# Performance work log

Hardware: AMD Instinct MI355X
Metric: run time of the kernel (lower is better)

## Reference

```python
import jax, jax.numpy as jnp
import numpy as np

B, N, RIN, ROUT, DEMB, FIN, FE, E, ITERS = 64, 128, 32, 64, 64, 64, 16, 65536, 3
NTOT = B * N


def gnn(x, edge_index, edge_feat, Ws, Wm, We, b):
    # edge-conditioned message passing: [NTOT, Fin] -> [NTOT, Fout]
    src, dst = edge_index[0], edge_index[1]
    msg = jax.nn.relu(x[src] @ Wm + edge_feat @ We)          # [E, Fout]
    agg = jax.ops.segment_sum(msg, dst, num_segments=x.shape[0])
    return jax.nn.relu(x @ Ws + agg + b)


def setup_inputs() -> dict:
    key = jax.random.key(0)
    ks = jax.random.split(key, 20)
    s = 0.1
    return {
        "x_r": jax.random.normal(ks[0], (NTOT, FIN), jnp.float32),
        "edge_index_r": jax.random.randint(ks[1], (2, E), 0, NTOT),
        "edge_feat_r": jax.random.normal(ks[2], (E, FE), jnp.float32),
        "x_p": jax.random.normal(ks[3], (NTOT, FIN), jnp.float32),
        "edge_index_p": jax.random.randint(ks[4], (2, E), 0, NTOT),
        "edge_feat_p": jax.random.normal(ks[5], (E, FE), jnp.float32),
        "r_mask": jnp.ones((B, N), dtype=bool),
        "p_mask": jnp.ones((B, N), dtype=bool),
        # gnn_1 params (FIN -> DEMB)
        "g1_Ws": jax.random.normal(ks[6], (FIN, DEMB)) * s,
        "g1_Wm": jax.random.normal(ks[7], (FIN, DEMB)) * s,
        "g1_We": jax.random.normal(ks[8], (FE, DEMB)) * s,
        "g1_b": jnp.zeros((DEMB,), jnp.float32),
        # gnn_2 params (RIN -> ROUT)
        "g2_Ws": jax.random.normal(ks[9], (RIN, ROUT)) * s,
        "g2_Wm": jax.random.normal(ks[10], (RIN, ROUT)) * s,
        "g2_We": jax.random.normal(ks[11], (FE, ROUT)) * s,
        "g2_b": jnp.zeros((ROUT,), jnp.float32),
        # consensus mlp (ROUT -> ROUT -> 1)
        "mlp_W1": jax.random.normal(ks[12], (ROUT, ROUT)) * s,
        "mlp_b1": jnp.zeros((ROUT,), jnp.float32),
        "mlp_W2": jax.random.normal(ks[13], (ROUT, 1)) * s,
        "mlp_b2": jnp.zeros((1,), jnp.float32),
    }


def reference(x_r, edge_index_r, edge_feat_r, x_p, edge_index_p, edge_feat_p,
              r_mask, p_mask,
              g1_Ws, g1_Wm, g1_We, g1_b,
              g2_Ws, g2_Wm, g2_We, g2_b,
              mlp_W1, mlp_b1, mlp_W2, mlp_b2):
    # node embeddings via gnn_1, then dense-batch to [B, N, DEMB]
    h_r = gnn(x_r, edge_index_r, edge_feat_r, g1_Ws, g1_Wm, g1_We, g1_b).reshape(B, N, DEMB)
    h_p = gnn(x_p, edge_index_p, edge_feat_p, g1_Ws, g1_Wm, g1_We, g1_b).reshape(B, N, DEMB)

    M_hat = jnp.einsum('brd,bpd->brp', h_r, h_p)             # [B, N_r, N_p]
    M_mask = r_mask[:, :, None] & p_mask[:, None, :]
    M_0 = jax.nn.softmax(M_hat, axis=-1).reshape(NTOT, N)    # packed (full mask)

    rkey = jax.random.key(42)
    for it in range(ITERS):
        M = jax.nn.softmax(M_hat, axis=-1)
        rf_r = jax.random.normal(jax.random.fold_in(rkey, it), (B, N, RIN), jnp.float32)
        rf_p = jnp.einsum('brp,bri->bpi', M, rf_r)           # M^T @ rand
        o_r = gnn(rf_r.reshape(NTOT, RIN), edge_index_r, edge_feat_r,
                  g2_Ws, g2_Wm, g2_We, g2_b).reshape(B, N, ROUT)
        o_p = gnn(rf_p.reshape(NTOT, RIN), edge_index_p, edge_feat_p,
                  g2_Ws, g2_Wm, g2_We, g2_b).reshape(B, N, ROUT)
        D = o_r[:, :, None, :] - o_p[:, None, :, :]          # [B, N_r, N_p, ROUT]
        upd = (jax.nn.relu(D @ mlp_W1 + mlp_b1) @ mlp_W2 + mlp_b2)[..., 0]
        M_hat = M_hat + jnp.where(M_mask, upd, 0.0)

    M_T = jax.nn.softmax(M_hat, axis=-1).reshape(NTOT, N)
    return (M_0, M_T)
```

## Files before the change

kernel.cpp:

```cpp
#include <hip/hip_runtime.h>

constexpr int kE = 65536, kNTOT = 8192;

__host__ __device__ __forceinline__ void tf_round(unsigned& x0, unsigned& x1, int r) {
  x0 += x1;
  x1 = (x1 << r) | (x1 >> (32 - r));
  x1 ^= x0;
}
__host__ __device__ __forceinline__ void tf2x32(unsigned k0, unsigned k1,
                                                unsigned& x0, unsigned& x1) {
  unsigned ks2 = k0 ^ k1 ^ 0x1BD11BDAu;
  x0 += k0; x1 += k1;
  tf_round(x0,x1,13); tf_round(x0,x1,15); tf_round(x0,x1,26); tf_round(x0,x1,6);
  x0 += k1; x1 += ks2 + 1u;
  tf_round(x0,x1,17); tf_round(x0,x1,29); tf_round(x0,x1,16); tf_round(x0,x1,24);
  x0 += ks2; x1 += k0 + 2u;
  tf_round(x0,x1,13); tf_round(x0,x1,15); tf_round(x0,x1,26); tf_round(x0,x1,6);
  x0 += k0; x1 += k1 + 3u;
  tf_round(x0,x1,17); tf_round(x0,x1,29); tf_round(x0,x1,16); tf_round(x0,x1,24);
  x0 += k1; x1 += ks2 + 4u;
  tf_round(x0,x1,13); tf_round(x0,x1,15); tf_round(x0,x1,26); tf_round(x0,x1,6);
  x0 += ks2; x1 += k0 + 5u;
}

__device__ __forceinline__ float bits_to_normal(unsigned bits) {
  float f = __uint_as_float((bits >> 9) | 0x3f800000u) - 1.0f;
  const float LO = -0.99999994f;
  float u = fmaf(f, 2.0f, LO);
  u = fmaxf(u, LO);
  float w = -log1pf(-u * u);
  float p;
  if (w < 5.0f) {
    w -= 2.5f;
    p = 2.81022636e-08f;
    p = fmaf(p, w, 3.43273939e-07f);
    p = fmaf(p, w, -3.5233877e-06f);
    p = fmaf(p, w, -4.39150654e-06f);
    p = fmaf(p, w, 0.00021858087f);
    p = fmaf(p, w, -0.00125372503f);
    p = fmaf(p, w, -0.00417768164f);
    p = fmaf(p, w, 0.246640727f);
    p = fmaf(p, w, 1.50140941f);
  } else {
    w = sqrtf(w) - 3.0f;
    p = -0.000200214257f;
    p = fmaf(p, w, 0.000100950558f);
    p = fmaf(p, w, 0.00134934322f);
    p = fmaf(p, w, -0.00367342844f);
    p = fmaf(p, w, 0.00573950773f);
    p = fmaf(p, w, -0.0076224613f);
    p = fmaf(p, w, 0.00943887047f);
    p = fmaf(p, w, 1.00167406f);
    p = fmaf(p, w, 2.83297682f);
  }
  return 1.41421356f * (p * u);
}

__device__ __forceinline__ float redmax32(float v) {
#pragma unroll
  for (int o = 16; o > 0; o >>= 1) v = fmaxf(v, __shfl_xor(v, o));
  return v;
}
__device__ __forceinline__ float redsum32(float v) {
#pragma unroll
  for (int o = 16; o > 0; o >>= 1) v += __shfl_xor(v, o);
  return v;
}

__global__ __launch_bounds__(256) void hist_kern(const int* __restrict__ eiR,
                                                 const int* __restrict__ eiP,
                                                 int* __restrict__ cntR,
                                                 int* __restrict__ cntP,
                                                 float* __restrict__ aggz) {
  int i = blockIdx.x * 256 + threadIdx.x;
  float4 z4 = make_float4(0.f, 0.f, 0.f, 0.f);
  float4* z = reinterpret_cast<float4*>(aggz) + i * 2;
  z[0] = z4; z[1] = z4;
  const int* ei = (i < kE) ? eiR : eiP;
  int* cnt = (i < kE) ? cntR : cntP;
  int e = i & (kE - 1);
  atomicAdd(&cnt[ei[kE + e]], 1);
}

__global__ __launch_bounds__(256) void scan_kern(const int* __restrict__ cntR,
                                                 int* __restrict__ rpR, int* __restrict__ offR,
                                                 const int* __restrict__ cntP,
                                                 int* __restrict__ rpP, int* __restrict__ offP) {
  const int* cnt = blockIdx.x ? cntP : cntR;
  int* rp = blockIdx.x ? rpP : rpR;
  int* off = blockIdx.x ? offP : offR;
  int t = threadIdx.x;
  int base = t * 32;
  int v[32];
#pragma unroll
  for (int i = 0; i < 32; ++i) v[i] = cnt[base + i];
  int sum = 0;
#pragma unroll
  for (int i = 0; i < 32; ++i) sum += v[i];
  int lane = t & 63, w = t >> 6;
  int incl = sum;
#pragma unroll
  for (int o = 1; o < 64; o <<= 1) {
    int y = __shfl_up(incl, o);
    if (lane >= o) incl += y;
  }
  __shared__ int wsum[4];
  if (lane == 63) wsum[w] = incl;
  __syncthreads();
  int woff = 0;
#pragma unroll
  for (int i = 0; i < 4; ++i) if (i < w) woff += wsum[i];
  int running = woff + incl - sum;
#pragma unroll
  for (int i = 0; i < 32; ++i) {
    rp[base + i] = running;
    off[base + i] = running;
    running += v[i];
  }
  if (t == 0) rp[kNTOT] = kE;
}

__global__ __launch_bounds__(256) void scatter_kern(
    const int* __restrict__ eiR, const int* __restrict__ eiP,
    int* __restrict__ offR, int* __restrict__ offP,
    int* __restrict__ permR, int* __restrict__ permP,
    int* __restrict__ srcsR, int* __restrict__ srcsP,
    int* __restrict__ dstsR, int* __restrict__ dstsP) {
  int i = blockIdx.x * 256 + threadIdx.x;
  const int* ei = (i < kE) ? eiR : eiP;
  int* off = (i < kE) ? offR : offP;
  int* perm = (i < kE) ? permR : permP;
  int* srcs = (i < kE) ? srcsR : srcsP;
  int* dsts = (i < kE) ? dstsR : dstsP;
  int e = i & (kE - 1);
  int dst = ei[kE + e];
  int pos = atomicAdd(&off[dst], 1);
  perm[pos] = e;
  srcs[pos] = ei[e];
  dsts[pos] = dst;
}

template <int KX>
__global__ __launch_bounds__(256) void msg_gemm(
    const float* __restrict__ xR, const float* __restrict__ efR,
    const int* __restrict__ srcsR, const int* __restrict__ permR,
    const int* __restrict__ dstsR, float* __restrict__ aggR,
    const float* __restrict__ xP, const float* __restrict__ efP,
    const int* __restrict__ srcsP, const int* __restrict__ permP,
    const int* __restrict__ dstsP, float* __restrict__ aggP,
    const float* __restrict__ Wm, const float* __restrict__ We) {
  constexpr int KT = KX + 16;
  constexpr int SA_ROWS = (KT > 64) ? KT : 64;
  __shared__ float sA[SA_ROWS][68];
  __shared__ float sW[KT][68];
  __shared__ int sDst[64];
  bool isP = blockIdx.x >= 1024;
  const float* x = isP ? xP : xR;
  const float* ef = isP ? efP : efR;
  const int* srcs = isP ? srcsP : srcsR;
  const int* perm = isP ? permP : permR;
  const int* dsts = isP ? dstsP : dstsR;
  float* agg = isP ? aggP : aggR;
  int i0 = (blockIdx.x & 1023) * 64;
  int t = threadIdx.x;
#pragma unroll
  for (int idx = 0; idx < KT * 64 / 1024; ++idx) {
    int q = t * 4 + idx * 1024;
    int k = q >> 6, j = q & 63;
    const float* sp = (k < KX) ? (Wm + k * 64 + j) : (We + (k - KX) * 64 + j);
    float4 v = *reinterpret_cast<const float4*>(sp);
    *reinterpret_cast<float4*>(&sW[k][j]) = v;
  }
  if (t < 64) sDst[t] = dsts[i0 + t];
#pragma unroll
  for (int idx = 0; idx < KT * 64 / 1024; ++idx) {
    int q = t * 4 + idx * 1024;
    int r = q / KT;
    int k = q % KT;
    const float* rptr = (k < KX) ? (x + (size_t)srcs[i0 + r] * KX + k)
                                 : (ef + (size_t)perm[i0 + r] * 16 + (k - KX));
    float4 v = *reinterpret_cast<const float4*>(rptr);
    sA[k + 0][r] = v.x; sA[k + 1][r] = v.y; sA[k + 2][r] = v.z; sA[k + 3][r] = v.w;
  }
  __syncthreads();
  int tn = (t & 15) * 4;
  int tj = (t >> 4) * 4;
  float acc[4][4] = {};
#pragma unroll 8
  for (int k = 0; k < KT; ++k) {
    float4 a = *reinterpret_cast<const float4*>(&sA[k][tn]);
    float4 b = *reinterpret_cast<const float4*>(&sW[k][tj]);
    acc[0][0] = fmaf(a.x, b.x, acc[0][0]); acc[0][1] = fmaf(a.x, b.y, acc[0][1]);
    acc[0][2] = fmaf(a.x, b.z, acc[0][2]); acc[0][3] = fmaf(a.x, b.w, acc[0][3]);
    acc[1][0] = fmaf(a.y, b.x, acc[1][0]); acc[1][1] = fmaf(a.y, b.y, acc[1][1]);
    acc[1][2] = fmaf(a.y, b.z, acc[1][2]); acc[1][3] = fmaf(a.y, b.w, acc[1][3]);
    acc[2][0] = fmaf(a.z, b.x, acc[2][0]); acc[2][1] = fmaf(a.z, b.y, acc[2][1]);
    acc[2][2] = fmaf(a.z, b.z, acc[2][2]); acc[2][3] = fmaf(a.z, b.w, acc[2][3]);
    acc[3][0] = fmaf(a.w, b.x, acc[3][0]); acc[3][1] = fmaf(a.w, b.y, acc[3][1]);
    acc[3][2] = fmaf(a.w, b.z, acc[3][2]); acc[3][3] = fmaf(a.w, b.w, acc[3][3]);
  }
  __syncthreads();
#pragma unroll
  for (int i = 0; i < 4; ++i) {
    sA[tn + i][tj + 0] = fmaxf(acc[i][0], 0.f);
    sA[tn + i][tj + 1] = fmaxf(acc[i][1], 0.f);
    sA[tn + i][tj + 2] = fmaxf(acc[i][2], 0.f);
    sA[tn + i][tj + 3] = fmaxf(acc[i][3], 0.f);
  }
  __syncthreads();
  int col = t & 63;
  int r0l = (t >> 6) * 16;
  float run = 0.f;
  int rd = sDst[r0l];
#pragma unroll
  for (int r = 0; r < 16; ++r) {
    int d = sDst[r0l + r];
    if (d != rd) {
      unsafeAtomicAdd(&agg[(size_t)rd * 64 + col], run);
      run = 0.f; rd = d;
    }
    run += sA[r0l + r][col];
  }
  unsafeAtomicAdd(&agg[(size_t)rd * 64 + col], run);
}

__global__ __launch_bounds__(256) void node1_gemm(
    const float* __restrict__ xR, float* __restrict__ aggR, float* __restrict__ hR,
    const float* __restrict__ xP, float* __restrict__ aggP, float* __restrict__ hP,
    const float* __restrict__ Ws, const float* __restrict__ bias) {
  __shared__ float sX[64][68];
  __shared__ float sW[64][68];
  bool isP = blockIdx.x >= 128;
  const float* x = isP ? xP : xR;
  float* agg = isP ? aggP : aggR;
  float* h = isP ? hP : hR;
  int n0 = (blockIdx.x & 127) * 64;
  int t = threadIdx.x;
#pragma unroll
  for (int idx = 0; idx < 4; ++idx) {
    int q = t * 4 + idx * 1024;
    int k = q >> 6, j = q & 63;
    *reinterpret_cast<float4*>(&sW[k][j]) = *reinterpret_cast<const float4*>(Ws + q);
    float4 v = *reinterpret_cast<const float4*>(x + (size_t)n0 * 64 + q);
    sX[j + 0][k] = v.x; sX[j + 1][k] = v.y; sX[j + 2][k] = v.z; sX[j + 3][k] = v.w;
  }
  __syncthreads();
  int tn = (t & 15) * 4, tj = (t >> 4) * 4;
  float acc[4][4] = {};
#pragma unroll 8
  for (int k = 0; k < 64; ++k) {
    float4 a = *reinterpret_cast<const float4*>(&sX[k][tn]);
    float4 b = *reinterpret_cast<const float4*>(&sW[k][tj]);
    acc[0][0] = fmaf(a.x, b.x, acc[0][0]); acc[0][1] = fmaf(a.x, b.y, acc[0][1]);
    acc[0][2] = fmaf(a.x, b.z, acc[0][2]); acc[0][3] = fmaf(a.x, b.w, acc[0][3]);
    acc[1][0] = fmaf(a.y, b.x, acc[1][0]); acc[1][1] = fmaf(a.y, b.y, acc[1][1]);
    acc[1][2] = fmaf(a.y, b.z, acc[1][2]); acc[1][3] = fmaf(a.y, b.w, acc[1][3]);
    acc[2][0] = fmaf(a.z, b.x, acc[2][0]); acc[2][1] = fmaf(a.z, b.y, acc[2][1]);
    acc[2][2] = fmaf(a.z, b.z, acc[2][2]); acc[2][3] = fmaf(a.z, b.w, acc[2][3]);
    acc[3][0] = fmaf(a.w, b.x, acc[3][0]); acc[3][1] = fmaf(a.w, b.y, acc[3][1]);
    acc[3][2] = fmaf(a.w, b.z, acc[3][2]); acc[3][3] = fmaf(a.w, b.w, acc[3][3]);
  }
  float4 bv = *reinterpret_cast<const float4*>(bias + tj);
  float4 z4 = make_float4(0.f, 0.f, 0.f, 0.f);
#pragma unroll
  for (int i = 0; i < 4; ++i) {
    int n = n0 + tn + i;
    float4 g = *reinterpret_cast<const float4*>(&agg[(size_t)n * 64 + tj]);
    *reinterpret_cast<float4*>(&agg[(size_t)n * 64 + tj]) = z4;
    float4 o;
    o.x = fmaxf(acc[i][0] + g.x + bv.x, 0.f);
    o.y = fmaxf(acc[i][1] + g.y + bv.y, 0.f);
    o.z = fmaxf(acc[i][2] + g.z + bv.z, 0.f);
    o.w = fmaxf(acc[i][3] + g.w + bv.w, 0.f);
    *reinterpret_cast<float4*>(&h[(size_t)n * 64 + tj]) = o;
  }
}

__global__ __launch_bounds__(256) void mhat_soft(
    const float* __restrict__ hR, const float* __restrict__ hP,
    float* __restrict__ Mhat, float* __restrict__ Msoft, float* __restrict__ M0out,
    float* __restrict__ rfr, unsigned fk0, unsigned fk1) {
  __shared__ float hr[16][66];
  __shared__ float hp[128][66];
  int gid = blockIdx.x, t = threadIdx.x;
  int gtid = (gid << 8) + t;
#pragma unroll
  for (int q = 0; q < 2; ++q) {
    unsigned i = (unsigned)gtid + (unsigned)q * 131072u;
    unsigned a0 = 0u, a1 = i;
    tf2x32(fk0, fk1, a0, a1);
    rfr[i] = bits_to_normal(a0 ^ a1);
  }
  int b = gid >> 3, r0 = (gid & 7) * 16;
  const float* hrG = hR + ((size_t)(b * 128 + r0)) * 64;
  {
    int q = t * 4; int r = q >> 6, d = q & 63;
    float4 v = *reinterpret_cast<const float4*>(hrG + q);
    hr[r][d] = v.x; hr[r][d + 1] = v.y; hr[r][d + 2] = v.z; hr[r][d + 3] = v.w;
  }
  const float* hpG = hP + (size_t)b * 128 * 64;
#pragma unroll
  for (int rep = 0; rep < 8; ++rep) {
    int q = (rep * 256 + t) * 4; int p = q >> 6, d = q & 63;
    float4 v = *reinterpret_cast<const float4*>(hpG + q);
    hp[p][d] = v.x; hp[p][d + 1] = v.y; hp[p][d + 2] = v.z; hp[p][d + 3] = v.w;
  }
  __syncthreads();
  int tx = t & 31, ty = t >> 5;
  float acc[2][4] = {};
  for (int d = 0; d < 64; ++d) {
    float a0 = hr[ty][d], a1 = hr[ty + 8][d];
    float q0 = hp[tx][d], q1 = hp[tx + 32][d], q2 = hp[tx + 64][d], q3 = hp[tx + 96][d];
    acc[0][0] = fmaf(a0, q0, acc[0][0]); acc[0][1] = fmaf(a0, q1, acc[0][1]);
    acc[0][2] = fmaf(a0, q2, acc[0][2]); acc[0][3] = fmaf(a0, q3, acc[0][3]);
    acc[1][0] = fmaf(a1, q0, acc[1][0]); acc[1][1] = fmaf(a1, q1, acc[1][1]);
    acc[1][2] = fmaf(a1, q2, acc[1][2]); acc[1][3] = fmaf(a1, q3, acc[1][3]);
  }
#pragma unroll
  for (int ii = 0; ii < 2; ++ii) {
    int r = r0 + ty + 8 * ii;
    float* mrow = Mhat + ((size_t)(b * 128 + r)) * 128;
    mrow[tx] = acc[ii][0]; mrow[tx + 32] = acc[ii][1];
    mrow[tx + 64] = acc[ii][2]; mrow[tx + 96] = acc[ii][3];
    float mx = redmax32(fmaxf(fmaxf(acc[ii][0], acc[ii][1]), fmaxf(acc[ii][2], acc[ii][3])));
    float e0 = __expf(acc[ii][0] - mx), e1 = __expf(acc[ii][1] - mx);
    float e2 = __expf(acc[ii][2] - mx), e3 = __expf(acc[ii][3] - mx);
    float inv = 1.0f / redsum32(e0 + e1 + e2 + e3);
    float* srow = Msoft + ((size_t)(b * 128 + r)) * 128;
    srow[tx] = e0 * inv; srow[tx + 32] = e1 * inv;
    srow[tx + 64] = e2 * inv; srow[tx + 96] = e3 * inv;
    float* orow = M0out + ((size_t)(b * 128 + r)) * 128;
    orow[tx] = e0 * inv; orow[tx + 32] = e1 * inv;
    orow[tx + 64] = e2 * inv; orow[tx + 96] = e3 * inv;
  }
}

__global__ __launch_bounds__(256) void rfp_kern(
    const float* __restrict__ Msoft, const float* __restrict__ rfr,
    float* __restrict__ rfp) {
  __shared__ float rr[128][36];
  int b = blockIdx.x >> 3, p0 = (blockIdx.x & 7) * 16;
  int t = threadIdx.x;
  const float* rfG = rfr + (size_t)b * 4096;
#pragma unroll
  for (int rep = 0; rep < 4; ++rep) {
    int q = (rep * 256 + t) * 4; int r = q >> 5, i = q & 31;
    float4 v = *reinterpret_cast<const float4*>(rfG + q);
    rr[r][i] = v.x; rr[r][i + 1] = v.y; rr[r][i + 2] = v.z; rr[r][i + 3] = v.w;
  }
  __syncthreads();
  int pl = t & 15, ih = (t >> 4) * 2;
  int p = p0 + pl;
  const float* Mcol = Msoft + (size_t)b * 16384 + p;
  float a0 = 0.f, a1 = 0.f;
#pragma unroll 8
  for (int r = 0; r < 128; ++r) {
    float m = Mcol[(size_t)r * 128];
    a0 = fmaf(m, rr[r][ih], a0);
    a1 = fmaf(m, rr[r][ih + 1], a1);
  }
  float* dst = rfp + ((size_t)(b * 128 + p)) * 32 + ih;
  dst[0] = a0; dst[1] = a1;
}

__global__ __launch_bounds__(256) void node2u_gemm(
    const float* __restrict__ rfR, float* __restrict__ aggR, float* __restrict__ uR,
    const float* __restrict__ rfP, float* __restrict__ aggP, float* __restrict__ uP,
    const float* __restrict__ Ws2, const float* __restrict__ g2b,
    const float* __restrict__ W1, const float* __restrict__ b1) {
  __shared__ float sRF[32][68];
  __shared__ float sW2[32][68];
  __shared__ float sW1[64][68];
  __shared__ float sO[64][68];
  bool isP = blockIdx.x >= 128;
  const float* rf = isP ? rfP : rfR;
  float* agg = isP ? aggP : aggR;
  float* u = isP ? uP : uR;
  int n0 = (blockIdx.x & 127) * 64;
  int t = threadIdx.x;
#pragma unroll
  for (int idx = 0; idx < 4; ++idx) {
    int q = t * 4 + idx * 1024;
    *reinterpret_cast<float4*>(&sW1[q >> 6][q & 63]) = *reinterpret_cast<const float4*>(W1 + q);
  }
#pragma unroll
  for (int idx = 0; idx < 2; ++idx) {
    int q = t * 4 + idx * 1024;
    *reinterpret_cast<float4*>(&sW2[q >> 6][q & 63]) = *reinterpret_cast<const float4*>(Ws2 + q);
    int r = q >> 5, kk = q & 31;
    float4 v = *reinterpret_cast<const float4*>(rf + (size_t)(n0 + r) * 32 + kk);
    sRF[kk][r] = v.x; sRF[kk + 1][r] = v.y; sRF[kk + 2][r] = v.z; sRF[kk + 3][r] = v.w;
  }
  __syncthreads();
  int tn = (t & 15) * 4, tj = (t >> 4) * 4;
  float acc[4][4] = {};
#pragma unroll 8
  for (int k = 0; k < 32; ++k) {
    float4 a = *reinterpret_cast<const float4*>(&sRF[k][tn]);
    float4 b = *reinterpret_cast<const float4*>(&sW2[k][tj]);
    acc[0][0] = fmaf(a.x, b.x, acc[0][0]); acc[0][1] = fmaf(a.x, b.y, acc[0][1]);
    acc[0][2] = fmaf(a.x, b.z, acc[0][2]); acc[0][3] = fmaf(a.x, b.w, acc[0][3]);
    acc[1][0] = fmaf(a.y, b.x, acc[1][0]); acc[1][1] = fmaf(a.y, b.y, acc[1][1]);
    acc[1][2] = fmaf(a.y, b.z, acc[1][2]); acc[1][3] = fmaf(a.y, b.w, acc[1][3]);
    acc[2][0] = fmaf(a.z, b.x, acc[2][0]); acc[2][1] = fmaf(a.z, b.y, acc[2][1]);
    acc[2][2] = fmaf(a.z, b.z, acc[2][2]); acc[2][3] = fmaf(a.z, b.w, acc[2][3]);
    acc[3][0] = fmaf(a.w, b.x, acc[3][0]); acc[3][1] = fmaf(a.w, b.y, acc[3][1]);
    acc[3][2] = fmaf(a.w, b.z, acc[3][2]); acc[3][3] = fmaf(a.w, b.w, acc[3][3]);
  }
  float4 bg = *reinterpret_cast<const float4*>(g2b + tj);
  float4 z4 = make_float4(0.f, 0.f, 0.f, 0.f);
#pragma unroll
  for (int i = 0; i < 4; ++i) {
    int n = n0 + tn + i;
    float4 g = *reinterpret_cast<const float4*>(&agg[(size_t)n * 64 + tj]);
    *reinterpret_cast<float4*>(&agg[(size_t)n * 64 + tj]) = z4;
    sO[tj + 0][tn + i] = fmaxf(acc[i][0] + g.x + bg.x, 0.f);
    sO[tj + 1][tn + i] = fmaxf(acc[i][1] + g.y + bg.y, 0.f);
    sO[tj + 2][tn + i] = fmaxf(acc[i][2] + g.z + bg.z, 0.f);
    sO[tj + 3][tn + i] = fmaxf(acc[i][3] + g.w + bg.w, 0.f);
  }
  __syncthreads();
  float acc2[4][4] = {};
#pragma unroll 8
  for (int k = 0; k < 64; ++k) {
    float4 a = *reinterpret_cast<const float4*>(&sO[k][tn]);
    float4 b = *reinterpret_cast<const float4*>(&sW1[k][tj]);
    acc2[0][0] = fmaf(a.x, b.x, acc2[0][0]); acc2[0][1] = fmaf(a.x, b.y, acc2[0][1]);
    acc2[0][2] = fmaf(a.x, b.z, acc2[0][2]); acc2[0][3] = fmaf(a.x, b.w, acc2[0][3]);
    acc2[1][0] = fmaf(a.y, b.x, acc2[1][0]); acc2[1][1] = fmaf(a.y, b.y, acc2[1][1]);
    acc2[1][2] = fmaf(a.y, b.z, acc2[1][2]); acc2[1][3] = fmaf(a.y, b.w, acc2[1][3]);
    acc2[2][0] = fmaf(a.z, b.x, acc2[2][0]); acc2[2][1] = fmaf(a.z, b.y, acc2[2][1]);
    acc2[2][2] = fmaf(a.z, b.z, acc2[2][2]); acc2[2][3] = fmaf(a.z, b.w, acc2[2][3]);
    acc2[3][0] = fmaf(a.w, b.x, acc2[3][0]); acc2[3][1] = fmaf(a.w, b.y, acc2[3][1]);
    acc2[3][2] = fmaf(a.w, b.z, acc2[3][2]); acc2[3][3] = fmaf(a.w, b.w, acc2[3][3]);
  }
  float4 b1v = make_float4(0.f, 0.f, 0.f, 0.f);
  if (!isP) b1v = *reinterpret_cast<const float4*>(b1 + tj);
#pragma unroll
  for (int i = 0; i < 4; ++i) {
    int n = n0 + tn + i;
    float4 o;
    o.x = acc2[i][0] + b1v.x; o.y = acc2[i][1] + b1v.y;
    o.z = acc2[i][2] + b1v.z; o.w = acc2[i][3] + b1v.w;
    *reinterpret_cast<float4*>(&u[(size_t)n * 64 + tj]) = o;
  }
}

__global__ __launch_bounds__(256) void upd_soft(
    const float* __restrict__ uR, const float* __restrict__ uP,
    const float* __restrict__ W2, const float* __restrict__ b2p,
    float* __restrict__ Mhat, float* __restrict__ softDst,
    int writeMhat, float* __restrict__ rfr, int doRng,
    unsigned fk0, unsigned fk1) {
  __shared__ float sur[16][66];
  __shared__ float sup[128][66];
  __shared__ float sw2[64];
  int gid = blockIdx.x, t = threadIdx.x;
  int b = gid >> 3, r0 = (gid & 7) * 16;
  const float* urG = uR + ((size_t)(b * 128 + r0)) * 64;
  {
    int q = t * 4; int r = q >> 6, d = q & 63;
    float4 v = *reinterpret_cast<const float4*>(urG + q);
    sur[r][d] = v.x; sur[r][d + 1] = v.y; sur[r][d + 2] = v.z; sur[r][d + 3] = v.w;
  }
  const float* upG = uP + (size_t)b * 128 * 64;
#pragma unroll
  for (int rep = 0; rep < 8; ++rep) {
    int q = (rep * 256 + t) * 4; int p = q >> 6, d = q & 63;
    float4 v = *reinterpret_cast<const float4*>(upG + q);
    sup[p][d] = v.x; sup[p][d + 1] = v.y; sup[p][d + 2] = v.z; sup[p][d + 3] = v.w;
  }
  if (t < 64) sw2[t] = W2[t];
  __syncthreads();
  int tx = t & 31, ty = t >> 5;
  float acc[2][4] = {};
  for (int j = 0; j < 64; ++j) {
    float w2v = sw2[j];
    float a0 = sur[ty][j], a1 = sur[ty + 8][j];
    float q0 = sup[tx][j], q1 = sup[tx + 32][j], q2 = sup[tx + 64][j], q3 = sup[tx + 96][j];
    acc[0][0] = fmaf(fmaxf(a0 - q0, 0.f), w2v, acc[0][0]);
    acc[0][1] = fmaf(fmaxf(a0 - q1, 0.f), w2v, acc[0][1]);
    acc[0][2] = fmaf(fmaxf(a0 - q2, 0.f), w2v, acc[0][2]);
    acc[0][3] = fmaf(fmaxf(a0 - q3, 0.f), w2v, acc[0][3]);
    acc[1][0] = fmaf(fmaxf(a1 - q0, 0.f), w2v, acc[1][0]);
    acc[1][1] = fmaf(fmaxf(a1 - q1, 0.f), w2v, acc[1][1]);
    acc[1][2] = fmaf(fmaxf(a1 - q2, 0.f), w2v, acc[1][2]);
    acc[1][3] = fmaf(fmaxf(a1 - q3, 0.f), w2v, acc[1][3]);
  }
  float b2v = b2p[0];
#pragma unroll
  for (int ii = 0; ii < 2; ++ii) {
    int r = r0 + ty + 8 * ii;
    float* mrow = Mhat + ((size_t)(b * 128 + r)) * 128;
    float m0 = mrow[tx] + acc[ii][0] + b2v;
    float m1 = mrow[tx + 32] + acc[ii][1] + b2v;
    float m2 = mrow[tx + 64] + acc[ii][2] + b2v;
    float m3 = mrow[tx + 96] + acc[ii][3] + b2v;
    if (writeMhat) {
      mrow[tx] = m0; mrow[tx + 32] = m1; mrow[tx + 64] = m2; mrow[tx + 96] = m3;
    }
    float mx = redmax32(fmaxf(fmaxf(m0, m1), fmaxf(m2, m3)));
    float e0 = __expf(m0 - mx), e1 = __expf(m1 - mx);
    float e2 = __expf(m2 - mx), e3 = __expf(m3 - mx);
    float inv = 1.0f / redsum32(e0 + e1 + e2 + e3);
    float* srow = softDst + ((size_t)(b * 128 + r)) * 128;
    srow[tx] = e0 * inv; srow[tx + 32] = e1 * inv;
    srow[tx + 64] = e2 * inv; srow[tx + 96] = e3 * inv;
  }
  if (doRng) {
    int gtid = (gid << 8) + t;
#pragma unroll
    for (int q = 0; q < 2; ++q) {
      unsigned i = (unsigned)gtid + (unsigned)q * 131072u;
      unsigned a0 = 0u, a1 = i;
      tf2x32(fk0, fk1, a0, a1);
      rfr[i] = bits_to_normal(a0 ^ a1);
    }
  }
}

extern "C" void kernel_launch(void* const* d_in, const int* in_sizes, int n_in,
                              void* d_out, int out_size, void* d_ws, size_t ws_size,
                              hipStream_t stream) {
  (void)in_sizes; (void)n_in; (void)out_size; (void)ws_size;
  const float* x_r  = (const float*)d_in[0];
  const int*   ei_r = (const int*)d_in[1];
  const float* ef_r = (const float*)d_in[2];
  const float* x_p  = (const float*)d_in[3];
  const int*   ei_p = (const int*)d_in[4];
  const float* ef_p = (const float*)d_in[5];
  const float* g1_Ws = (const float*)d_in[8];
  const float* g1_Wm = (const float*)d_in[9];
  const float* g1_We = (const float*)d_in[10];
  const float* g1_b  = (const float*)d_in[11];
  const float* g2_Ws = (const float*)d_in[12];
  const float* g2_Wm = (const float*)d_in[13];
  const float* g2_We = (const float*)d_in[14];
  const float* g2_b  = (const float*)d_in[15];
  const float* W1 = (const float*)d_in[16];
  const float* b1 = (const float*)d_in[17];
  const float* W2 = (const float*)d_in[18];
  const float* b2 = (const float*)d_in[19];
  float* out = (float*)d_out;

  float* ws = (float*)d_ws;
  float* h_r   = ws;
  float* h_p   = h_r + 524288;
  float* Mhat  = h_p + 524288;
  float* Msoft = Mhat + 1048576;
  float* rfr   = Msoft + 1048576;
  float* rfp   = rfr + 262144;
  float* u_r   = rfp + 262144;
  float* u_p   = u_r + 524288;
  float* agg_r = u_p + 524288;
  float* agg_p = agg_r + 524288;
  int* ib      = (int*)(agg_p + 524288);
  int* cnt_r  = ib;
  int* cnt_p  = cnt_r + 8192;
  int* off_r  = cnt_p + 8192;
  int* off_p  = off_r + 8192;
  int* rp_r   = off_p + 8192;
  int* rp_p   = rp_r + 8193;
  int* perm_r = rp_p + 8193;
  int* perm_p = perm_r + 65536;
  int* srcs_r = perm_p + 65536;
  int* srcs_p = srcs_r + 65536;
  int* dsts_r = srcs_p + 65536;
  int* dsts_p = dsts_r + 65536;

  unsigned fk0[3], fk1[3];
  for (int it = 0; it < 3; ++it) {
    unsigned a = 0u, c = (unsigned)it;
    tf2x32(0u, 42u, a, c);
    fk0[it] = a; fk1[it] = c;
  }

  hipMemsetAsync(cnt_r, 0, 2 * 8192 * sizeof(int), stream);
  hist_kern<<<512, 256, 0, stream>>>(ei_r, ei_p, cnt_r, cnt_p, agg_r);
  scan_kern<<<2, 256, 0, stream>>>(cnt_r, rp_r, off_r, cnt_p, rp_p, off_p);
  scatter_kern<<<512, 256, 0, stream>>>(ei_r, ei_p, off_r, off_p,
                                        perm_r, perm_p, srcs_r, srcs_p,
                                        dsts_r, dsts_p);

  msg_gemm<64><<<2048, 256, 0, stream>>>(x_r, ef_r, srcs_r, perm_r, dsts_r, agg_r,
                                         x_p, ef_p, srcs_p, perm_p, dsts_p, agg_p,
                                         g1_Wm, g1_We);
  node1_gemm<<<256, 256, 0, stream>>>(x_r, agg_r, h_r, x_p, agg_p, h_p, g1_Ws, g1_b);
  mhat_soft<<<512, 256, 0, stream>>>(h_r, h_p, Mhat, Msoft, out, rfr, fk0[0], fk1[0]);

  for (int it = 0; it < 3; ++it) {
    rfp_kern<<<512, 256, 0, stream>>>(Msoft, rfr, rfp);
    msg_gemm<32><<<2048, 256, 0, stream>>>(rfr, ef_r, srcs_r, perm_r, dsts_r, agg_r,
                                           rfp, ef_p, srcs_p, perm_p, dsts_p, agg_p,
                                           g2_Wm, g2_We);
    node2u_gemm<<<256, 256, 0, stream>>>(rfr, agg_r, u_r, rfp, agg_p, u_p,
                                         g2_Ws, g2_b, W1, b1);
    int last = (it == 2);
    upd_soft<<<512, 256, 0, stream>>>(u_r, u_p, W2, b2, Mhat,
                                      last ? (out + 1048576) : Msoft,
                                      !last,
                                      rfr, !last,
                                      fk0[it < 2 ? it + 1 : 0], fk1[it < 2 ? it + 1 : 0]);
  }
}
```

Before: 316.6 us.

## Fuse M^T·rand projection into softmax kernels via atomics, drop Msoft buffer

Result: slower. 629.6 us (+98.8%).

```diff
diff --git a/kernel.cpp b/kernel.cpp
--- a/kernel.cpp
+++ b/kernel.cpp
@@ -67,33 +67,60 @@
   return v;
 }
 
+__device__ __forceinline__ void rfp_tail(float* sm, int b, int r0, int t,
+                                         float* __restrict__ rfr,
+                                         float* __restrict__ rfp,
+                                         unsigned fk0, unsigned fk1) {
+  unsigned base = (unsigned)(b * 4096 + r0 * 32);
+#pragma unroll
+  for (int q = 0; q < 2; ++q) {
+    int il = t * 2 + q;
+    unsigned a0 = 0u, a1 = base + (unsigned)il;
+    tf2x32(fk0, fk1, a0, a1);
+    float nv = bits_to_normal(a0 ^ a1);
+    sm[2112 + (il >> 5) * 33 + (il & 31)] = nv;
+    rfr[base + il] = nv;
+  }
+  __syncthreads();
+  int p = t >> 1, ih = (t & 1) * 16;
+  float acc[16] = {};
+#pragma unroll
+  for (int lr = 0; lr < 16; ++lr) {
+    float m = sm[lr * 132 + p];
+    const float* rrr = &sm[2112 + lr * 33 + ih];
+#pragma unroll
+    for (int i = 0; i < 16; ++i) acc[i] = fmaf(m, rrr[i], acc[i]);
+  }
+  float* dst = rfp + ((size_t)(b * 128 + p)) * 32 + ih;
+#pragma unroll
+  for (int i = 0; i < 16; ++i) unsafeAtomicAdd(dst + i, acc[i]);
+}
+
 __global__ __launch_bounds__(256) void hist_kern(const int* __restrict__ eiR,
                                                  const int* __restrict__ eiP,
-                                                 int* __restrict__ cntR,
-                                                 int* __restrict__ cntP,
-                                                 float* __restrict__ aggz) {
+                                                 int* __restrict__ offR,
+                                                 int* __restrict__ offP,
+                                                 float* __restrict__ aggz,
+                                                 float* __restrict__ rfpz) {
   int i = blockIdx.x * 256 + threadIdx.x;
   float4 z4 = make_float4(0.f, 0.f, 0.f, 0.f);
   float4* z = reinterpret_cast<float4*>(aggz) + i * 2;
   z[0] = z4; z[1] = z4;
+  reinterpret_cast<float2*>(rfpz)[i] = make_float2(0.f, 0.f);
   const int* ei = (i < kE) ? eiR : eiP;
-  int* cnt = (i < kE) ? cntR : cntP;
+  int* off = (i < kE) ? offR : offP;
   int e = i & (kE - 1);
-  atomicAdd(&cnt[ei[kE + e]], 1);
-}
-
-__global__ __launch_bounds__(256) void scan_kern(const int* __restrict__ cntR,
-                                                 int* __restrict__ rpR, int* __restrict__ offR,
-                                                 const int* __restrict__ cntP,
-                                                 int* __restrict__ rpP, int* __restrict__ offP) {
-  const int* cnt = blockIdx.x ? cntP : cntR;
-  int* rp = blockIdx.x ? rpP : rpR;
+  atomicAdd(&off[ei[kE + e]], 1);
+}
+
+__global__ __launch_bounds__(256) void scan_kern(int* __restrict__ offR,
+                                                 int* __restrict__ offP) {
   int* off = blockIdx.x ? offP : offR;
   int t = threadIdx.x;
   int base = t * 32;
   int v[32];
 #pragma unroll
-  for (int i = 0; i < 32; ++i) v[i] = cnt[base + i];
+  for (int i = 0; i < 32; ++i) v[i] = off[base + i];
   int sum = 0;
 #pragma unroll
   for (int i = 0; i < 32; ++i) sum += v[i];
@@ -113,11 +140,9 @@
   int running = woff + incl - sum;
 #pragma unroll
   for (int i = 0; i < 32; ++i) {
-    rp[base + i] = running;
     off[base + i] = running;
     running += v[i];
   }
-  if (t == 0) rp[kNTOT] = kE;
 }
 
 __global__ __launch_bounds__(256) void scatter_kern(
@@ -202,10 +227,9 @@
   __syncthreads();
 #pragma unroll
   for (int i = 0; i < 4; ++i) {
-    sA[tn + i][tj + 0] = fmaxf(acc[i][0], 0.f);
-    sA[tn + i][tj + 1] = fmaxf(acc[i][1], 0.f);
-    sA[tn + i][tj + 2] = fmaxf(acc[i][2], 0.f);
-    sA[tn + i][tj + 3] = fmaxf(acc[i][3], 0.f);
+    *reinterpret_cast<float4*>(&sA[tn + i][tj]) =
+        make_float4(fmaxf(acc[i][0], 0.f), fmaxf(acc[i][1], 0.f),
+                    fmaxf(acc[i][2], 0.f), fmaxf(acc[i][3], 0.f));
   }
   __syncthreads();
   int col = t & 63;
@@ -278,44 +302,40 @@
 
 __global__ __launch_bounds__(256) void mhat_soft(
     const float* __restrict__ hR, const float* __restrict__ hP,
-    float* __restrict__ Mhat, float* __restrict__ Msoft, float* __restrict__ M0out,
-    float* __restrict__ rfr, unsigned fk0, unsigned fk1) {
-  __shared__ float hr[16][66];
-  __shared__ float hp[128][66];
+    float* __restrict__ Mhat, float* __restrict__ M0out,
+    float* __restrict__ rfr, float* __restrict__ rfp,
+    unsigned fk0, unsigned fk1) {
+  __shared__ float sm[9504];
   int gid = blockIdx.x, t = threadIdx.x;
-  int gtid = (gid << 8) + t;
-#pragma unroll
-  for (int q = 0; q < 2; ++q) {
-    unsigned i = (unsigned)gtid + (unsigned)q * 131072u;
-    unsigned a0 = 0u, a1 = i;
-    tf2x32(fk0, fk1, a0, a1);
-    rfr[i] = bits_to_normal(a0 ^ a1);
-  }
   int b = gid >> 3, r0 = (gid & 7) * 16;
   const float* hrG = hR + ((size_t)(b * 128 + r0)) * 64;
   {
     int q = t * 4; int r = q >> 6, d = q & 63;
     float4 v = *reinterpret_cast<const float4*>(hrG + q);
-    hr[r][d] = v.x; hr[r][d + 1] = v.y; hr[r][d + 2] = v.z; hr[r][d + 3] = v.w;
+    sm[r * 66 + d] = v.x; sm[r * 66 + d + 1] = v.y;
+    sm[r * 66 + d + 2] = v.z; sm[r * 66 + d + 3] = v.w;
   }
   const float* hpG = hP + (size_t)b * 128 * 64;
 #pragma unroll
   for (int rep = 0; rep < 8; ++rep) {
     int q = (rep * 256 + t) * 4; int p = q >> 6, d = q & 63;
     float4 v = *reinterpret_cast<const float4*>(hpG + q);
-    hp[p][d] = v.x; hp[p][d + 1] = v.y; hp[p][d + 2] = v.z; hp[p][d + 3] = v.w;
+    sm[1056 + p * 66 + d] = v.x; sm[1056 + p * 66 + d + 1] = v.y;
+    sm[1056 + p * 66 + d + 2] = v.z; sm[1056 + p * 66 + d + 3] = v.w;
   }
   __syncthreads();
   int tx = t & 31, ty = t >> 5;
   float acc[2][4] = {};
   for (int d = 0; d < 64; ++d) {
-    float a0 = hr[ty][d], a1 = hr[ty + 8][d];
-    float q0 = hp[tx][d], q1 = hp[tx + 32][d], q2 = hp[tx + 64][d], q3 = hp[tx + 96][d];
+    float a0 = sm[ty * 66 + d], a1 = sm[(ty + 8) * 66 + d];
+    float q0 = sm[1056 + tx * 66 + d], q1 = sm[1056 + (tx + 32) * 66 + d];
+    float q2 = sm[1056 + (tx + 64) * 66 + d], q3 = sm[1056 + (tx + 96) * 66 + d];
     acc[0][0] = fmaf(a0, q0, acc[0][0]); acc[0][1] = fmaf(a0, q1, acc[0][1]);
     acc[0][2] = fmaf(a0, q2, acc[0][2]); acc[0][3] = fmaf(a0, q3, acc[0][3]);
     acc[1][0] = fmaf(a1, q0, acc[1][0]); acc[1][1] = fmaf(a1, q1, acc[1][1]);
     acc[1][2] = fmaf(a1, q2, acc[1][2]); acc[1][3] = fmaf(a1, q3, acc[1][3]);
   }
+  float prob[2][4];
 #pragma unroll
   for (int ii = 0; ii < 2; ++ii) {
     int r = r0 + ty + 8 * ii;
@@ -326,46 +346,25 @@
     float e0 = __expf(acc[ii][0] - mx), e1 = __expf(acc[ii][1] - mx);
     float e2 = __expf(acc[ii][2] - mx), e3 = __expf(acc[ii][3] - mx);
     float inv = 1.0f / redsum32(e0 + e1 + e2 + e3);
-    float* srow = Msoft + ((size_t)(b * 128 + r)) * 128;
-    srow[tx] = e0 * inv; srow[tx + 32] = e1 * inv;
-    srow[tx + 64] = e2 * inv; srow[tx + 96] = e3 * inv;
+    prob[ii][0] = e0 * inv; prob[ii][1] = e1 * inv;
+    prob[ii][2] = e2 * inv; prob[ii][3] = e3 * inv;
     float* orow = M0out + ((size_t)(b * 128 + r)) * 128;
-    orow[tx] = e0 * inv; orow[tx + 32] = e1 * inv;
-    orow[tx + 64] = e2 * inv; orow[tx + 96] = e3 * inv;
-  }
-}
-
-__global__ __launch_bounds__(256) void rfp_kern(
-    const float* __restrict__ Msoft, const float* __restrict__ rfr,
-    float* __restrict__ rfp) {
-  __shared__ float rr[128][36];
-  int b = blockIdx.x >> 3, p0 = (blockIdx.x & 7) * 16;
-  int t = threadIdx.x;
-  const float* rfG = rfr + (size_t)b * 4096;
-#pragma unroll
-  for (int rep = 0; rep < 4; ++rep) {
-    int q = (rep * 256 + t) * 4; int r = q >> 5, i = q & 31;
-    float4 v = *reinterpret_cast<const float4*>(rfG + q);
-    rr[r][i] = v.x; rr[r][i + 1] = v.y; rr[r][i + 2] = v.z; rr[r][i + 3] = v.w;
-  }
-  __syncthreads();
-  int pl = t & 15, ih = (t >> 4) * 2;
-  int p = p0 + pl;
-  const float* Mcol = Msoft + (size_t)b * 16384 + p;
-  float a0 = 0.f, a1 = 0.f;
-#pragma unroll 8
-  for (int r = 0; r < 128; ++r) {
-    float m = Mcol[(size_t)r * 128];
-    a0 = fmaf(m, rr[r][ih], a0);
-    a1 = fmaf(m, rr[r][ih + 1], a1);
-  }
-  float* dst = rfp + ((size_t)(b * 128 + p)) * 32 + ih;
-  dst[0] = a0; dst[1] = a1;
+    orow[tx] = prob[ii][0]; orow[tx + 32] = prob[ii][1];
+    orow[tx + 64] = prob[ii][2]; orow[tx + 96] = prob[ii][3];
+  }
+  __syncthreads();
+#pragma unroll
+  for (int ii = 0; ii < 2; ++ii) {
+    int lr = ty + 8 * ii;
+    sm[lr * 132 + tx] = prob[ii][0]; sm[lr * 132 + tx + 32] = prob[ii][1];
+    sm[lr * 132 + tx + 64] = prob[ii][2]; sm[lr * 132 + tx + 96] = prob[ii][3];
+  }
+  rfp_tail(sm, b, r0, t, rfr, rfp, fk0, fk1);
 }
 
 __global__ __launch_bounds__(256) void node2u_gemm(
     const float* __restrict__ rfR, float* __restrict__ aggR, float* __restrict__ uR,
-    const float* __restrict__ rfP, float* __restrict__ aggP, float* __restrict__ uP,
+    float* __restrict__ rfP, float* __restrict__ aggP, float* __restrict__ uP,
     const float* __restrict__ Ws2, const float* __restrict__ g2b,
     const float* __restrict__ W1, const float* __restrict__ b1) {
   __shared__ float sRF[32][68];
@@ -392,6 +391,14 @@
     sRF[kk][r] = v.x; sRF[kk + 1][r] = v.y; sRF[kk + 2][r] = v.z; sRF[kk + 3][r] = v.w;
   }
   __syncthreads();
+  if (isP) {
+    float4 z4 = make_float4(0.f, 0.f, 0.f, 0.f);
+#pragma unroll
+    for (int idx = 0; idx < 2; ++idx) {
+      int q = t * 4 + idx * 1024;
+      *reinterpret_cast<float4*>(rfP + (size_t)n0 * 32 + q) = z4;
+    }
+  }
   int tn = (t & 15) * 4, tj = (t >> 4) * 4;
   float acc[4][4] = {};
 #pragma unroll 8
@@ -449,35 +456,36 @@
 __global__ __launch_bounds__(256) void upd_soft(
     const float* __restrict__ uR, const float* __restrict__ uP,
     const float* __restrict__ W2, const float* __restrict__ b2p,
-    float* __restrict__ Mhat, float* __restrict__ softDst,
-    int writeMhat, float* __restrict__ rfr, int doRng,
+    float* __restrict__ Mhat, float* __restrict__ outLast, int last,
+    float* __restrict__ rfr, float* __restrict__ rfp,
     unsigned fk0, unsigned fk1) {
-  __shared__ float sur[16][66];
-  __shared__ float sup[128][66];
-  __shared__ float sw2[64];
+  __shared__ float sm[9568];
   int gid = blockIdx.x, t = threadIdx.x;
   int b = gid >> 3, r0 = (gid & 7) * 16;
   const float* urG = uR + ((size_t)(b * 128 + r0)) * 64;
   {
     int q = t * 4; int r = q >> 6, d = q & 63;
     float4 v = *reinterpret_cast<const float4*>(urG + q);
-    sur[r][d] = v.x; sur[r][d + 1] = v.y; sur[r][d + 2] = v.z; sur[r][d + 3] = v.w;
+    sm[r * 66 + d] = v.x; sm[r * 66 + d + 1] = v.y;
+    sm[r * 66 + d + 2] = v.z; sm[r * 66 + d + 3] = v.w;
   }
   const float* upG = uP + (size_t)b * 128 * 64;
 #pragma unroll
   for (int rep = 0; rep < 8; ++rep) {
     int q = (rep * 256 + t) * 4; int p = q >> 6, d = q & 63;
     float4 v = *reinterpret_cast<const float4*>(upG + q);
-    sup[p][d] = v.x; sup[p][d + 1] = v.y; sup[p][d + 2] = v.z; sup[p][d + 3] = v.w;
-  }
-  if (t < 64) sw2[t] = W2[t];
+    sm[1056 + p * 66 + d] = v.x; sm[1056 + p * 66 + d + 1] = v.y;
+    sm[1056 + p * 66 + d + 2] = v.z; sm[1056 + p * 66 + d + 3] = v.w;
+  }
+  if (t < 64) sm[9504 + t] = W2[t];
   __syncthreads();
   int tx = t & 31, ty = t >> 5;
   float acc[2][4] = {};
   for (int j = 0; j < 64; ++j) {
-    float w2v = sw2[j];
-    float a0 = sur[ty][j], a1 = sur[ty + 8][j];
-    float q0 = sup[tx][j], q1 = sup[tx + 32][j], q2 = sup[tx + 64][j], q3 = sup[tx + 96][j];
+    float w2v = sm[9504 + j];
+    float a0 = sm[ty * 66 + j], a1 = sm[(ty + 8) * 66 + j];
+    float q0 = sm[1056 + tx * 66 + j], q1 = sm[1056 + (tx + 32) * 66 + j];
+    float q2 = sm[1056 + (tx + 64) * 66 + j], q3 = sm[1056 + (tx + 96) * 66 + j];
     acc[0][0] = fmaf(fmaxf(a0 - q0, 0.f), w2v, acc[0][0]);
     acc[0][1] = fmaf(fmaxf(a0 - q1, 0.f), w2v, acc[0][1]);
     acc[0][2] = fmaf(fmaxf(a0 - q2, 0.f), w2v, acc[0][2]);
@@ -488,6 +496,7 @@
     acc[1][3] = fmaf(fmaxf(a1 - q3, 0.f), w2v, acc[1][3]);
   }
   float b2v = b2p[0];
+  float prob[2][4];
 #pragma unroll
   for (int ii = 0; ii < 2; ++ii) {
     int r = r0 + ty + 8 * ii;
@@ -496,27 +505,30 @@
     float m1 = mrow[tx + 32] + acc[ii][1] + b2v;
     float m2 = mrow[tx + 64] + acc[ii][2] + b2v;
     float m3 = mrow[tx + 96] + acc[ii][3] + b2v;
-    if (writeMhat) {
+    if (!last) {
       mrow[tx] = m0; mrow[tx + 32] = m1; mrow[tx + 64] = m2; mrow[tx + 96] = m3;
     }
     float mx = redmax32(fmaxf(fmaxf(m0, m1), fmaxf(m2, m3)));
     float e0 = __expf(m0 - mx), e1 = __expf(m1 - mx);
     float e2 = __expf(m2 - mx), e3 = __expf(m3 - mx);
     float inv = 1.0f / redsum32(e0 + e1 + e2 + e3);
-    float* srow = softDst + ((size_t)(b * 128 + r)) * 128;
-    srow[tx] = e0 * inv; srow[tx + 32] = e1 * inv;
-    srow[tx + 64] = e2 * inv; srow[tx + 96] = e3 * inv;
-  }
-  if (doRng) {
-    int gtid = (gid << 8) + t;
-#pragma unroll
-    for (int q = 0; q < 2; ++q) {
-      unsigned i = (unsigned)gtid + (unsigned)q * 131072u;
-      unsigned a0 = 0u, a1 = i;
-      tf2x32(fk0, fk1, a0, a1);
-      rfr[i] = bits_to_normal(a0 ^ a1);
+    prob[ii][0] = e0 * inv; prob[ii][1] = e1 * inv;
+    prob[ii][2] = e2 * inv; prob[ii][3] = e3 * inv;
+    if (last) {
+      float* orow = outLast + ((size_t)(b * 128 + r)) * 128;
+      orow[tx] = prob[ii][0]; orow[tx + 32] = prob[ii][1];
+      orow[tx + 64] = prob[ii][2]; orow[tx + 96] = prob[ii][3];
     }
   }
+  if (last) return;
+  __syncthreads();
+#pragma unroll
+  for (int ii = 0; ii < 2; ++ii) {
+    int lr = ty + 8 * ii;
+    sm[lr * 132 + tx] = prob[ii][0]; sm[lr * 132 + tx + 32] = prob[ii][1];
+    sm[lr * 132 + tx + 64] = prob[ii][2]; sm[lr * 132 + tx + 96] = prob[ii][3];
+  }
+  rfp_tail(sm, b, r0, t, rfr, rfp, fk0, fk1);
 }
 
 extern "C" void kernel_launch(void* const* d_in, const int* in_sizes, int n_in,
@@ -547,21 +559,16 @@
   float* h_r   = ws;
   float* h_p   = h_r + 524288;
   float* Mhat  = h_p + 524288;
-  float* Msoft = Mhat + 1048576;
-  float* rfr   = Msoft + 1048576;
+  float* rfr   = Mhat + 1048576;
   float* rfp   = rfr + 262144;
   float* u_r   = rfp + 262144;
   float* u_p   = u_r + 524288;
   float* agg_r = u_p + 524288;
   float* agg_p = agg_r + 524288;
   int* ib      = (int*)(agg_p + 524288);
-  int* cnt_r  = ib;
-  int* cnt_p  = cnt_r + 8192;
-  int* off_r  = cnt_p + 8192;
+  int* off_r  = ib;
   int* off_p  = off_r + 8192;
-  int* rp_r   = off_p + 8192;
-  int* rp_p   = rp_r + 8193;
-  int* perm_r = rp_p + 8193;
+  int* perm_r = off_p + 8192;
   int* perm_p = perm_r + 65536;
   int* srcs_r = perm_p + 65536;
   int* srcs_p = srcs_r + 65536;
@@ -575,9 +582,9 @@
     fk0[it] = a; fk1[it] = c;
   }
 
-  hipMemsetAsync(cnt_r, 0, 2 * 8192 * sizeof(int), stream);
-  hist_kern<<<512, 256, 0, stream>>>(ei_r, ei_p, cnt_r, cnt_p, agg_r);
-  scan_kern<<<2, 256, 0, stream>>>(cnt_r, rp_r, off_r, cnt_p, rp_p, off_p);
+  hipMemsetAsync(off_r, 0, 2 * 8192 * sizeof(int), stream);
+  hist_kern<<<512, 256, 0, stream>>>(ei_r, ei_p, off_r, off_p, agg_r, rfp);
+  scan_kern<<<2, 256, 0, stream>>>(off_r, off_p);
   scatter_kern<<<512, 256, 0, stream>>>(ei_r, ei_p, off_r, off_p,
                                         perm_r, perm_p, srcs_r, srcs_p,
                                         dsts_r, dsts_p);
@@ -586,10 +593,9 @@
                                          x_p, ef_p, srcs_p, perm_p, dsts_p, agg_p,
                                          g1_Wm, g1_We);
   node1_gemm<<<256, 256, 0, stream>>>(x_r, agg_r, h_r, x_p, agg_p, h_p, g1_Ws, g1_b);
-  mhat_soft<<<512, 256, 0, stream>>>(h_r, h_p, Mhat, Msoft, out, rfr, fk0[0], fk1[0]);
+  mhat_soft<<<512, 256, 0, stream>>>(h_r, h_p, Mhat, out, rfr, rfp, fk0[0], fk1[0]);
 
   for (int it = 0; it < 3; ++it) {
-    rfp_kern<<<512, 256, 0, stream>>>(Msoft, rfr, rfp);
     msg_gemm<32><<<2048, 256, 0, stream>>>(rfr, ef_r, srcs_r, perm_r, dsts_r, agg_r,
                                            rfp, ef_p, srcs_p, perm_p, dsts_p, agg_p,
                                            g2_Wm, g2_We);
@@ -597,9 +603,7 @@
                                          g2_Ws, g2_b, W1, b1);
     int last = (it == 2);
     upd_soft<<<512, 256, 0, stream>>>(u_r, u_p, W2, b2, Mhat,
-                                      last ? (out + 1048576) : Msoft,
-                                      !last,
-                                      rfr, !last,
-                                      fk0[it < 2 ? it + 1 : 0], fk1[it < 2 ? it + 1 : 0]);
-  }
-}
+                                      out + 1048576, last, rfr, rfp,
+                                      fk0[last ? 0 : it + 1], fk1[last ? 0 : it + 1]);
+  }
+}
```
